# Optimization experiments

Measured on AMD Instinct MI355X. Metric: run time of the kernel, lower is better.

The kernel has to match this reference:

```python
import jax, jax.numpy as jnp
import numpy as np

B, C, W, H = 1024, 1, 128, 128
NUM_IDS = 64
MARGIN = 0.3


def setup_inputs() -> dict:
    key = jax.random.key(0)
    k1, k2 = jax.random.split(key)
    inputs = jax.random.normal(k1, (B, C, W, H), dtype=jnp.float32)
    targets = jax.random.randint(k2, (B,), 0, NUM_IDS, dtype=jnp.int32)
    return {"inputs": inputs, "targets": targets}


def _dc_align(anchor, other):
    # Batched cross-attention alignment (DCModuleOptimized assumption):
    # modi = softmax(anchor @ other^T / sqrt(h)) @ other, per sample.
    h = anchor.shape[-1]
    scale = 1.0 / jnp.sqrt(jnp.asarray(h, anchor.dtype))
    att = jax.nn.softmax(jnp.einsum('bij,bkj->bik', anchor, other) * scale, axis=-1)
    return jnp.einsum('bik,bkj->bij', att, other)


def reference(inputs, targets):
    b, c, w, h = inputs.shape
    x = inputs.reshape(b, -1)                      # (n, d); requires c == 1 downstream
    n = b
    # Pairwise Euclidean distances, stable clamp as in torch code
    sq = jnp.sum(x * x, axis=1)                    # (n,)
    dist = sq[:, None] + sq[None, :] - 2.0 * (x @ x.T)
    dist = jnp.sqrt(jnp.clip(dist, 1e-12, None))   # (n, n)
    mask = targets[:, None] == targets[None, :]    # (n, n) same-identity mask
    # Vectorized hard mining (replaces the per-row Python loop)
    NEG = jnp.asarray(-1e30, dist.dtype)
    POS = jnp.asarray(1e30, dist.dtype)
    hp_idx = jnp.argmax(jnp.where(mask, dist, NEG), axis=1)   # hardest positive per row
    hn_idx = jnp.argmin(jnp.where(mask, POS, dist), axis=1)   # hardest negative per row
    anchor = x.reshape(b, w, h)
    h_pos = anchor[hp_idx]                         # (b, w, h) gathered hard positives
    h_neg = anchor[hn_idx]                         # (b, w, h) gathered hard negatives
    # DC module applied over the whole batch at once
    modi_pos = _dc_align(anchor, h_pos)
    modi_neg = _dc_align(anchor, h_neg)
    dap = anchor.reshape(b, -1) - modi_pos.reshape(b, -1)
    dan = anchor.reshape(b, -1) - modi_neg.reshape(b, -1)
    dist_ap = jnp.sqrt(jnp.sum(dap * dap, axis=1))
    dist_an = jnp.sqrt(jnp.sum(dan * dan, axis=1))
    # MarginRankingLoss with y = 1: mean(relu(dist_ap - dist_an + margin))
    loss = jnp.mean(jax.nn.relu(dist_ap - dist_an + MARGIN))
    return loss
```

## Files before the change

### kernel.cpp

```cpp
#include <hip/hip_runtime.h>
#include <stdint.h>

#define NSAMP 1024
#define D 16384
#define WH 128
#define MARGIN 0.3f
#define SCALE 0.08838834764831845f
#define RSCALE 11.313708498984761f
#define MARG 0.03f
#define NKS 16
#define NTILE 36

typedef unsigned int uint;
typedef unsigned short ushort_t;

typedef __attribute__((ext_vector_type(8))) short bf16x8;
typedef __attribute__((ext_vector_type(4))) float f32x4;

__device__ __forceinline__ float bf2f(unsigned short b) {
    return __uint_as_float(((uint)b) << 16);
}
__device__ __forceinline__ unsigned short f2bf(float f) {
    uint u = __float_as_uint(f);
    u += 0x7fffu + ((u >> 16) & 1u);
    return (unsigned short)(u >> 16);
}
__device__ __forceinline__ void gload_lds16(const void* g, void* l) {
    __builtin_amdgcn_global_load_lds(
        (const __attribute__((address_space(1))) uint32_t*)g,
        (__attribute__((address_space(3))) uint32_t*)l, 16, 0, 0);
}
__device__ __forceinline__ int lds_off(int row, int col) {
    return row * 256 + ((((col >> 3) ^ (row & 15)) << 4) | ((col & 7) << 1));
}

__global__ __launch_bounds__(256) void k_norms_hi(const float* __restrict__ x,
                                                  float* __restrict__ sq,
                                                  ushort_t* __restrict__ xhi) {
    int b = blockIdx.x;
    int tid = threadIdx.x;
    const float* xr = x + (size_t)b * D;
    ushort_t* hr = xhi + (size_t)b * D;
    float s = 0.f;
    #pragma unroll
    for (int m = 0; m < 16; ++m) {
        int e = m * 1024 + tid * 4;
        float4 v = *(const float4*)(xr + e);
        s += v.x * v.x + v.y * v.y + v.z * v.z + v.w * v.w;
        ushort4 h;
        h.x = f2bf(v.x); h.y = f2bf(v.y); h.z = f2bf(v.z); h.w = f2bf(v.w);
        *(ushort4*)(hr + e) = h;
    }
    for (int off = 32; off; off >>= 1) s += __shfl_down(s, off, 64);
    __shared__ float red[4];
    if ((tid & 63) == 0) red[tid >> 6] = s;
    __syncthreads();
    if (tid == 0) sq[b] = red[0] + red[1] + red[2] + red[3];
}

__global__ __launch_bounds__(256) void k_gram_hi(const ushort_t* __restrict__ xhi,
                                                 float* __restrict__ Gp) {
    int n = blockIdx.x;
    int r8 = n & 7;
    int m = n >> 3;
    int h = m / 36;
    int t = m - 36 * h;
    int ks = r8 + 8 * h;
    int bi = 0, rem = t;
    while (rem >= 8 - bi) { rem -= 8 - bi; ++bi; }
    int bj = bi + rem;
    int i0 = bi * 128, j0 = bj * 128;
    int kstart = ks * (D / NKS);

    int tid = threadIdx.x;
    int w = tid >> 6, lane = tid & 63;
    int wm = w & 1, wn = w >> 1;
    int quad = lane >> 4, m16 = lane & 15;
    int srow = lane >> 2, sseg = lane & 3;
    int swseg = sseg ^ ((srow >> 1) & 3);
    int rsw = (quad ^ ((m16 >> 1) & 3)) << 3;

    __shared__ __align__(16) ushort_t A_s[2][128 * 32];
    __shared__ __align__(16) ushort_t B_s[2][128 * 32];

    f32x4 acc[4][4];
    #pragma unroll
    for (int ii = 0; ii < 4; ++ii)
        #pragma unroll
        for (int jj = 0; jj < 4; ++jj)
            acc[ii][jj] = (f32x4){0.f, 0.f, 0.f, 0.f};

    const size_t Abase = (size_t)i0 * D;
    const size_t Bbase = (size_t)j0 * D;

    auto stage = [&](int s) {
        int bsel = s & 1;
        int k0 = kstart + s * 32;
        #pragma unroll
        for (int c = 0; c < 2; ++c) {
            int r = w * 32 + c * 16 + srow;
            size_t go = (size_t)r * D + k0 + swseg * 8;
            int lo = (w * 32 + c * 16) * 32;
            gload_lds16(xhi + Abase + go, &A_s[bsel][lo]);
            gload_lds16(xhi + Bbase + go, &B_s[bsel][lo]);
        }
    };
    auto compute = [&](int bsel) {
        bf16x8 ah[4], bh[4];
        #pragma unroll
        for (int ii = 0; ii < 4; ++ii) {
            int ar = wm * 64 + ii * 16 + m16;
            ah[ii] = *(const bf16x8*)&A_s[bsel][ar * 32 + rsw];
        }
        #pragma unroll
        for (int jj = 0; jj < 4; ++jj) {
            int br = wn * 64 + jj * 16 + m16;
            bh[jj] = *(const bf16x8*)&B_s[bsel][br * 32 + rsw];
        }
        #pragma unroll
        for (int ii = 0; ii < 4; ++ii)
            #pragma unroll
            for (int jj = 0; jj < 4; ++jj)
                acc[ii][jj] = __builtin_amdgcn_mfma_f32_16x16x32_bf16(ah[ii], bh[jj], acc[ii][jj], 0, 0, 0);
    };

    stage(0);
    for (int kb = 0; kb < 31; ++kb) {
        stage(kb + 1);
        asm volatile("s_waitcnt vmcnt(4)" ::: "memory");
        __builtin_amdgcn_sched_barrier(0);
        __builtin_amdgcn_s_barrier();
        compute(kb & 1);
        __builtin_amdgcn_s_barrier();
    }
    asm volatile("s_waitcnt vmcnt(0)" ::: "memory");
    __builtin_amdgcn_sched_barrier(0);
    __builtin_amdgcn_s_barrier();
    compute(1);

    float* Gb = Gp + ((size_t)(t * NKS + ks) << 14);
    #pragma unroll
    for (int ii = 0; ii < 4; ++ii)
        #pragma unroll
        for (int jj = 0; jj < 4; ++jj) {
            int rg = wm * 64 + ii * 16 + quad * 4;
            int cg = wn * 64 + jj * 16 + m16;
            #pragma unroll
            for (int r = 0; r < 4; ++r)
                Gb[(rg + r) * 128 + cg] = acc[ii][jj][r];
        }
}

__global__ __launch_bounds__(256) void k_fold_tri(const float* __restrict__ Gp,
                                                  float* __restrict__ G) {
    int t = blockIdx.x;
    int panel = blockIdx.y;
    int bi = 0, rem = t;
    while (rem >= 8 - bi) { rem -= 8 - bi; ++bi; }
    int bj = bi + rem;
    bool diag = (bi == bj);
    int tid = threadIdx.x;

    const float* P = Gp + (((size_t)t * NKS) << 14) + panel * 4096;

    float4 s[4];
    #pragma unroll
    for (int m = 0; m < 4; ++m)
        s[m] = *(const float4*)(P + (tid + 256 * m) * 4);
    #pragma unroll
    for (int p = 1; p < NKS; ++p) {
        const float* Pp = P + (((size_t)p) << 14);
        #pragma unroll
        for (int m = 0; m < 4; ++m) {
            float4 v = *(const float4*)(Pp + (tid + 256 * m) * 4);
            s[m].x += v.x; s[m].y += v.y; s[m].z += v.z; s[m].w += v.w;
        }
    }

    int i0 = bi * 128, j0 = bj * 128, r0 = panel * 32;
    __shared__ float ts[32][129];
    #pragma unroll
    for (int m = 0; m < 4; ++m) {
        int p4 = (tid + 256 * m) * 4;
        int lr = p4 >> 7, lc = p4 & 127;
        *(float4*)(&G[(size_t)(i0 + r0 + lr) * NSAMP + j0 + lc]) = s[m];
        if (!diag) {
            ts[lr][lc] = s[m].x; ts[lr][lc + 1] = s[m].y;
            ts[lr][lc + 2] = s[m].z; ts[lr][lc + 3] = s[m].w;
        }
    }
    if (diag) return;
    __syncthreads();
    int oc = tid >> 1, half = tid & 1;
    float4 o[4];
    #pragma unroll
    for (int k = 0; k < 4; ++k) {
        int rr = half * 16 + k * 4;
        o[k].x = ts[rr][oc]; o[k].y = ts[rr + 1][oc];
        o[k].z = ts[rr + 2][oc]; o[k].w = ts[rr + 3][oc];
    }
    float* Gm = &G[(size_t)(j0 + oc) * NSAMP + i0 + r0 + half * 16];
    #pragma unroll
    for (int k = 0; k < 4; ++k) *(float4*)(Gm + k * 4) = o[k];
}

__global__ __launch_bounds__(256) void k_select_fix(const float* __restrict__ G,
                                                    const float* __restrict__ sq,
                                                    const int* __restrict__ tgt,
                                                    const float* __restrict__ x,
                                                    const ushort_t* __restrict__ xhi,
                                                    int* __restrict__ hp,
                                                    int* __restrict__ hn,
                                                    float* __restrict__ dsq) {
    int i = blockIdx.x;
    int tid = threadIdx.x;
    float sqi = sq[i];
    int ti = tgt[i];
    float dloc[4]; bool sloc[4];
    float pv = -3.0e38f; int pj = 0x7FFFFFFF;
    float nv = 3.0e38f;  int nj = 0x7FFFFFFF;
    #pragma unroll
    for (int m = 0; m < 4; ++m) {
        int j = tid + 256 * m;
        float g = G[(size_t)i * NSAMP + j];
        float d = sqrtf(fmaxf(sqi + sq[j] - 2.f * g, 1e-12f));
        bool same = (tgt[j] == ti);
        dloc[m] = d; sloc[m] = same;
        float cp = same ? d : -1e30f;
        float cn = same ? 1e30f : d;
        if (cp > pv || (cp == pv && j < pj)) { pv = cp; pj = j; }
        if (cn < nv || (cn == nv && j < nj)) { nv = cn; nj = j; }
    }
    for (int off = 32; off; off >>= 1) {
        float opv = __shfl_down(pv, off, 64); int opj = __shfl_down(pj, off, 64);
        float onv = __shfl_down(nv, off, 64); int onj = __shfl_down(nj, off, 64);
        if (opv > pv || (opv == pv && opj < pj)) { pv = opv; pj = opj; }
        if (onv < nv || (onv == nv && onj < nj)) { nv = onv; nj = onj; }
    }
    __shared__ float spv[4], snv[4];
    __shared__ int spj[4], snj[4];
    __shared__ float bb[2];
    __shared__ int cc[2];
    if ((tid & 63) == 0) { int wv = tid >> 6; spv[wv] = pv; spj[wv] = pj; snv[wv] = nv; snj[wv] = nj; }
    __syncthreads();
    if (tid == 0) {
        for (int wv = 1; wv < 4; ++wv) {
            if (spv[wv] > pv || (spv[wv] == pv && spj[wv] < pj)) { pv = spv[wv]; pj = spj[wv]; }
            if (snv[wv] < nv || (snv[wv] == nv && snj[wv] < nj)) { nv = snv[wv]; nj = snj[wv]; }
        }
        hp[i] = pj; hn[i] = nj;
        dsq[i] = sqi; dsq[NSAMP + i] = sqi;
        bb[0] = pv; bb[1] = nv;
        cc[0] = 0; cc[1] = 0;
    }
    __syncthreads();
    {
        int lp = 0, ln = 0;
        #pragma unroll
        for (int m = 0; m < 4; ++m) {
            if (sloc[m] && dloc[m] >= bb[0] - MARG) lp++;
            if (!sloc[m] && dloc[m] <= bb[1] + MARG) ln++;
        }
        if (lp) atomicAdd(&cc[0], lp);
        if (ln) atomicAdd(&cc[1], ln);
    }
    __syncthreads();

    __shared__ int cand[32];
    __shared__ int ncand;
    __shared__ float bred[4];
    const float* xi = x + (size_t)i * D;
    const ushort_t* hi = xhi + (size_t)i * D;
    for (int type = 0; type < 2; ++type) {
        if (cc[type] <= 1) continue;
        if (tid == 0) ncand = 0;
        __syncthreads();
        float bd = bb[type];
        #pragma unroll
        for (int m = 0; m < 4; ++m) {
            int j = tid + 256 * m;
            bool fl = (type == 0) ? (sloc[m] && dloc[m] >= bd - MARG)
                                  : (!sloc[m] && dloc[m] <= bd + MARG);
            if (fl) { int k = atomicAdd(&ncand, 1); if (k < 32) cand[k] = j; }
        }
        __syncthreads();
        int nc = ncand < 32 ? ncand : 32;
        float bestv = (type == 0) ? -3.0e38f : 3.0e38f;
        int bestj = 0x7FFFFFFF;
        for (int c = 0; c < nc; ++c) {
            int j = cand[c];
            const float* xj = x + (size_t)j * D;
            const ushort_t* hj = xhi + (size_t)j * D;
            float corr = 0.f;
            #pragma unroll
            for (int m = 0; m < 16; ++m) {
                int k = m * 1024 + tid * 4;
                float4 xa = *(const float4*)(xi + k);
                float4 xb = *(const float4*)(xj + k);
                ushort4 ha = *(const ushort4*)(hi + k);
                ushort4 hb = *(const ushort4*)(hj + k);
                float a0 = bf2f(ha.x), a1 = bf2f(ha.y), a2 = bf2f(ha.z), a3 = bf2f(ha.w);
                float b0 = bf2f(hb.x), b1 = bf2f(hb.y), b2 = bf2f(hb.z), b3 = bf2f(hb.w);
                corr += a0 * (xb.x - b0) + (xa.x - a0) * b0;
                corr += a1 * (xb.y - b1) + (xa.y - a1) * b1;
                corr += a2 * (xb.z - b2) + (xa.z - a2) * b2;
                corr += a3 * (xb.w - b3) + (xa.w - a3) * b3;
            }
            for (int off = 32; off; off >>= 1) corr += __shfl_down(corr, off, 64);
            if ((tid & 63) == 0) bred[tid >> 6] = corr;
            __syncthreads();
            float cs = bred[0] + bred[1] + bred[2] + bred[3];
            float g = G[(size_t)i * NSAMP + j];
            float d2 = sqi + sq[j] - 2.f * (g + cs);
            float d = sqrtf(fmaxf(d2, 1e-12f));
            if (type == 0) {
                if (d > bestv || (d == bestv && j < bestj)) { bestv = d; bestj = j; }
            } else {
                if (d < bestv || (d == bestv && j < bestj)) { bestv = d; bestj = j; }
            }
            __syncthreads();
        }
        if (tid == 0 && nc > 0) { if (type == 0) hp[i] = bestj; else hn[i] = bestj; }
        __syncthreads();
    }
}

__global__ __launch_bounds__(256) void k_dc_mfma(const ushort_t* __restrict__ xhi,
                                                 const int* __restrict__ hp,
                                                 const int* __restrict__ hn,
                                                 float* __restrict__ dsq) {
    int b = blockIdx.x;
    int which = blockIdx.y;
    int oidx = (which == 0) ? hp[b] : hn[b];
    const ushort_t* Ag = xhi + (size_t)b * D;
    const ushort_t* Og = xhi + (size_t)oidx * D;

    __shared__ __align__(16) char smem[32768];

    int tid = threadIdx.x;
    int wv = tid >> 6, lane = tid & 63;
    int quad = lane >> 4, m16 = lane & 15;

    bf16x8 af[2][4];
    #pragma unroll
    for (int h = 0; h < 2; ++h) {
        int rt = h * 4 + wv;
        #pragma unroll
        for (int ks = 0; ks < 4; ++ks)
            af[h][ks] = *(const bf16x8*)(Ag + (rt * 16 + m16) * WH + ks * 32 + quad * 8);
    }

    {
        uint4 stg[8];
        #pragma unroll
        for (int k = 0; k < 8; ++k)
            stg[k] = *(const uint4*)((const char*)Og + (size_t)(tid + 256 * k) * 16);
        #pragma unroll
        for (int k = 0; k < 8; ++k) {
            int g = tid + 256 * k;
            *(uint4*)(smem + lds_off(g >> 4, (g & 15) * 8)) = stg[k];
        }
    }
    __syncthreads();

    f32x4 acc[2][8];
    #pragma unroll
    for (int h = 0; h < 2; ++h)
        #pragma unroll
        for (int ti = 0; ti < 8; ++ti)
            acc[h][ti] = (f32x4){0.f, 0.f, 0.f, 0.f};
    #pragma unroll
    for (int ks = 0; ks < 4; ++ks) {
        bf16x8 of[8];
        #pragma unroll
        for (int ti = 0; ti < 8; ++ti)
            of[ti] = *(const bf16x8*)(smem + lds_off(ti * 16 + m16, (ks * 4 + quad) * 8));
        #pragma unroll
        for (int h = 0; h < 2; ++h)
            #pragma unroll
            for (int ti = 0; ti < 8; ++ti)
                acc[h][ti] = __builtin_amdgcn_mfma_f32_16x16x32_bf16(of[ti], af[h][ks], acc[h][ti], 0, 0, 0);
    }

    int c0 = (tid & 31) * 4, h0 = (tid >> 5) * 16;
    uint4 trd[4][2];
    #pragma unroll
    for (int j = 0; j < 4; ++j)
        #pragma unroll
        for (int k = 0; k < 2; ++k)
            trd[j][k] = *(const uint4*)(smem + lds_off(c0 + j, h0 + 8 * k));
    __syncthreads();

    #pragma unroll
    for (int i = 0; i < 16; ++i) {
        uint v[4];
        #pragma unroll
        for (int j = 0; j < 4; ++j) {
            uint wo = ((const uint*)&trd[j][i >> 3])[(i >> 1) & 3];
            v[j] = (i & 1) ? (wo >> 16) : (wo & 0xffffu);
        }
        uint2 pk;
        pk.x = v[0] | (v[1] << 16);
        pk.y = v[2] | (v[3] << 16);
        *(uint2*)(smem + lds_off(h0 + i, c0)) = pk;
    }

    float tpart[2];
    bf16x8 pf[2][4];
    #pragma unroll
    for (int h = 0; h < 2; ++h) {
        float mx = -3.0e38f;
        #pragma unroll
        for (int ti = 0; ti < 8; ++ti)
            #pragma unroll
            for (int r = 0; r < 4; ++r) {
                float s = acc[h][ti][r] * SCALE;
                acc[h][ti][r] = s;
                mx = fmaxf(mx, s);
            }
        mx = fmaxf(mx, __shfl_xor(mx, 16, 64));
        mx = fmaxf(mx, __shfl_xor(mx, 32, 64));
        float sum = 0.f, tnum = 0.f;
        #pragma unroll
        for (int ti = 0; ti < 8; ++ti)
            #pragma unroll
            for (int r = 0; r < 4; ++r) {
                float s = acc[h][ti][r];
                float e = __expf(s - mx);
                acc[h][ti][r] = e;
                sum += e;
                tnum += s * e;
            }
        sum += __shfl_xor(sum, 16, 64);
        sum += __shfl_xor(sum, 32, 64);
        tnum += __shfl_xor(tnum, 16, 64);
        tnum += __shfl_xor(tnum, 32, 64);
        float inv = 1.f / sum;
        tpart[h] = 0.25f * tnum * inv;

        uint Ep[8][2];
        #pragma unroll
        for (int ti = 0; ti < 8; ++ti) {
            Ep[ti][0] = (uint)f2bf(acc[h][ti][0] * inv) |
                        ((uint)f2bf(acc[h][ti][1] * inv) << 16);
            Ep[ti][1] = (uint)f2bf(acc[h][ti][2] * inv) |
                        ((uint)f2bf(acc[h][ti][3] * inv) << 16);
        }
        int tih = quad >> 1;
        #pragma unroll
        for (int ks = 0; ks < 4; ++ks) {
            union { uint u[4]; bf16x8 v; } fr;
            #pragma unroll
            for (int k = 0; k < 4; ++k) {
                int src = (((quad << 1) + (k >> 1)) & 3) * 16 + m16;
                int a = __shfl((int)Ep[2 * ks + 0][k & 1], src, 64);
                int bsh = __shfl((int)Ep[2 * ks + 1][k & 1], src, 64);
                fr.u[k] = (uint)((tih == 0) ? a : bsh);
            }
            pf[h][ks] = fr.v;
        }
    }
    __syncthreads();

    #pragma unroll
    for (int h = 0; h < 2; ++h)
        #pragma unroll
        for (int tj = 0; tj < 8; ++tj)
            acc[h][tj] = (f32x4){0.f, 0.f, 0.f, 0.f};
    #pragma unroll
    for (int ks = 0; ks < 4; ++ks) {
        bf16x8 otf[8];
        #pragma unroll
        for (int tj = 0; tj < 8; ++tj)
            otf[tj] = *(const bf16x8*)(smem + lds_off(tj * 16 + m16, (ks * 4 + quad) * 8));
        #pragma unroll
        for (int h = 0; h < 2; ++h)
            #pragma unroll
            for (int tj = 0; tj < 8; ++tj)
                acc[h][tj] = __builtin_amdgcn_mfma_f32_16x16x32_bf16(pf[h][ks], otf[tj], acc[h][tj], 0, 0, 0);
    }

    float part = 0.f;
    #pragma unroll
    for (int h = 0; h < 2; ++h) {
        float m2 = 0.f;
        #pragma unroll
        for (int tj = 0; tj < 8; ++tj)
            #pragma unroll
            for (int r = 0; r < 4; ++r) {
                float mvv = acc[h][tj][r];
                m2 += mvv * mvv;
            }
        part += m2 - 2.f * RSCALE * tpart[h];
    }
    for (int off = 32; off; off >>= 1) part += __shfl_down(part, off, 64);
    if (lane == 0) atomicAdd(&dsq[which * NSAMP + b], part);
}

__global__ void k_loss(const float* __restrict__ dsq, float* __restrict__ out) {
    int tid = threadIdx.x;
    float s = 0.f;
    #pragma unroll
    for (int m = 0; m < 4; ++m) {
        int b = tid + 256 * m;
        float ap = sqrtf(fmaxf(dsq[b], 0.f));
        float an = sqrtf(fmaxf(dsq[NSAMP + b], 0.f));
        s += fmaxf(ap - an + MARGIN, 0.f);
    }
    for (int off = 32; off; off >>= 1) s += __shfl_down(s, off, 64);
    __shared__ float red[4];
    if ((tid & 63) == 0) red[tid >> 6] = s;
    __syncthreads();
    if (tid == 0) out[0] = (red[0] + red[1] + red[2] + red[3]) * (1.f / NSAMP);
}

extern "C" void kernel_launch(void* const* d_in, const int* in_sizes, int n_in,
                              void* d_out, int out_size, void* d_ws, size_t ws_size,
                              hipStream_t stream) {
    const float* x = (const float*)d_in[0];
    const int* tgt = (const int*)d_in[1];
    float* out = (float*)d_out;
    char* ws = (char*)d_ws;

    const size_t GPB = (size_t)NTILE * NKS * 65536;
    const size_t XB = (size_t)NSAMP * D * 2;
    const size_t GB1 = (size_t)NSAMP * NSAMP * 4;

    float* Gp = (float*)ws;
    ushort_t* xhi = (ushort_t*)(ws + GPB);
    float* G = (float*)(ws + GPB + XB);
    char* tail = ws + GPB + XB + GB1;
    float* sq = (float*)tail;
    float* dsq = sq + NSAMP;
    int* hp = (int*)(dsq + 2 * NSAMP);
    int* hn = hp + NSAMP;

    k_norms_hi<<<NSAMP, 256, 0, stream>>>(x, sq, xhi);
    k_gram_hi<<<NKS * NTILE, 256, 0, stream>>>(xhi, Gp);
    k_fold_tri<<<dim3(NTILE, 4), 256, 0, stream>>>(Gp, G);
    k_select_fix<<<NSAMP, 256, 0, stream>>>(G, sq, tgt, x, xhi, hp, hn, dsq);
    k_dc_mfma<<<dim3(NSAMP, 2), 256, 0, stream>>>(xhi, hp, hn, dsq);
    k_loss<<<1, 256, 0, stream>>>(dsq, out);
}
```

Baseline: 195.0 us.

## Fuse pos/neg DC alignment into one block and simplify gram pipeline

The DC alignment kernel now handles both the hardest-positive and the hardest-negative partner in one block. The anchor fragments are loaded once and reused, and the partner tile is staged directly into LDS with async global-to-LDS loads. The gram kernel's double-buffered loop is rewritten to use plain __syncthreads instead of explicit vmcnt waits, and both kernels raise wave priority around MFMA bursts with s_setprio. This halves the DC grid and removes redundant anchor loads, but the two partners are now processed serially within a block, so there is less parallelism. The gram loop may also lose some of its overlap between loads and compute.

```diff
diff --git a/kernel.cpp b/kernel.cpp
--- a/kernel.cpp
+++ b/kernel.cpp
@@ -93,9 +93,7 @@
     const size_t Abase = (size_t)i0 * D;
     const size_t Bbase = (size_t)j0 * D;
 
-    auto stage = [&](int s) {
-        int bsel = s & 1;
-        int k0 = kstart + s * 32;
+    auto stage = [&](int bsel, int k0) {
         #pragma unroll
         for (int c = 0; c < 2; ++c) {
             int r = w * 32 + c * 16 + srow;
@@ -117,26 +115,24 @@
             int br = wn * 64 + jj * 16 + m16;
             bh[jj] = *(const bf16x8*)&B_s[bsel][br * 32 + rsw];
         }
+        __builtin_amdgcn_s_setprio(1);
         #pragma unroll
         for (int ii = 0; ii < 4; ++ii)
             #pragma unroll
             for (int jj = 0; jj < 4; ++jj)
                 acc[ii][jj] = __builtin_amdgcn_mfma_f32_16x16x32_bf16(ah[ii], bh[jj], acc[ii][jj], 0, 0, 0);
+        __builtin_amdgcn_s_setprio(0);
     };
 
-    stage(0);
-    for (int kb = 0; kb < 31; ++kb) {
-        stage(kb + 1);
-        asm volatile("s_waitcnt vmcnt(4)" ::: "memory");
-        __builtin_amdgcn_sched_barrier(0);
-        __builtin_amdgcn_s_barrier();
-        compute(kb & 1);
-        __builtin_amdgcn_s_barrier();
-    }
-    asm volatile("s_waitcnt vmcnt(0)" ::: "memory");
-    __builtin_amdgcn_sched_barrier(0);
-    __builtin_amdgcn_s_barrier();
-    compute(1);
+    stage(0, kstart);
+    __syncthreads();
+    int buf = 0;
+    for (int kb = 0; kb < 32; ++kb) {
+        if (kb < 31) stage(buf ^ 1, kstart + (kb + 1) * 32);
+        compute(buf);
+        __syncthreads();
+        buf ^= 1;
+    }
 
     float* Gb = Gp + ((size_t)(t * NKS + ks) << 14);
     #pragma unroll
@@ -330,10 +326,8 @@
                                                  const int* __restrict__ hn,
                                                  float* __restrict__ dsq) {
     int b = blockIdx.x;
-    int which = blockIdx.y;
-    int oidx = (which == 0) ? hp[b] : hn[b];
     const ushort_t* Ag = xhi + (size_t)b * D;
-    const ushort_t* Og = xhi + (size_t)oidx * D;
+    int oidx[2] = {hp[b], hn[b]};
 
     __shared__ __align__(16) char smem[32768];
 
@@ -350,151 +344,163 @@
             af[h][ks] = *(const bf16x8*)(Ag + (rt * 16 + m16) * WH + ks * 32 + quad * 8);
     }
 
-    {
-        uint4 stg[8];
-        #pragma unroll
-        for (int k = 0; k < 8; ++k)
-            stg[k] = *(const uint4*)((const char*)Og + (size_t)(tid + 256 * k) * 16);
+    auto stage_O = [&](const ushort_t* Og) {
         #pragma unroll
         for (int k = 0; k < 8; ++k) {
-            int g = tid + 256 * k;
-            *(uint4*)(smem + lds_off(g >> 4, (g & 15) * 8)) = stg[k];
-        }
-    }
-    __syncthreads();
-
-    f32x4 acc[2][8];
-    #pragma unroll
-    for (int h = 0; h < 2; ++h)
-        #pragma unroll
-        for (int ti = 0; ti < 8; ++ti)
-            acc[h][ti] = (f32x4){0.f, 0.f, 0.f, 0.f};
-    #pragma unroll
-    for (int ks = 0; ks < 4; ++ks) {
-        bf16x8 of[8];
-        #pragma unroll
-        for (int ti = 0; ti < 8; ++ti)
-            of[ti] = *(const bf16x8*)(smem + lds_off(ti * 16 + m16, (ks * 4 + quad) * 8));
+            int p = tid + 256 * k;
+            int row = p >> 4, s = p & 15;
+            gload_lds16(Og + row * 128 + ((s ^ (row & 15)) << 3),
+                        smem + p * 16);
+        }
+    };
+
+    stage_O(xhi + (size_t)oidx[0] * D);
+    __syncthreads();
+
+    for (int which = 0; which < 2; ++which) {
+        f32x4 acc[2][8];
         #pragma unroll
         for (int h = 0; h < 2; ++h)
             #pragma unroll
             for (int ti = 0; ti < 8; ++ti)
-                acc[h][ti] = __builtin_amdgcn_mfma_f32_16x16x32_bf16(of[ti], af[h][ks], acc[h][ti], 0, 0, 0);
-    }
-
-    int c0 = (tid & 31) * 4, h0 = (tid >> 5) * 16;
-    uint4 trd[4][2];
-    #pragma unroll
-    for (int j = 0; j < 4; ++j)
-        #pragma unroll
-        for (int k = 0; k < 2; ++k)
-            trd[j][k] = *(const uint4*)(smem + lds_off(c0 + j, h0 + 8 * k));
-    __syncthreads();
-
-    #pragma unroll
-    for (int i = 0; i < 16; ++i) {
-        uint v[4];
-        #pragma unroll
-        for (int j = 0; j < 4; ++j) {
-            uint wo = ((const uint*)&trd[j][i >> 3])[(i >> 1) & 3];
-            v[j] = (i & 1) ? (wo >> 16) : (wo & 0xffffu);
-        }
-        uint2 pk;
-        pk.x = v[0] | (v[1] << 16);
-        pk.y = v[2] | (v[3] << 16);
-        *(uint2*)(smem + lds_off(h0 + i, c0)) = pk;
-    }
-
-    float tpart[2];
-    bf16x8 pf[2][4];
-    #pragma unroll
-    for (int h = 0; h < 2; ++h) {
-        float mx = -3.0e38f;
-        #pragma unroll
-        for (int ti = 0; ti < 8; ++ti)
-            #pragma unroll
-            for (int r = 0; r < 4; ++r) {
-                float s = acc[h][ti][r] * SCALE;
-                acc[h][ti][r] = s;
-                mx = fmaxf(mx, s);
+                acc[h][ti] = (f32x4){0.f, 0.f, 0.f, 0.f};
+        #pragma unroll
+        for (int ks = 0; ks < 4; ++ks) {
+            bf16x8 of[8];
+            #pragma unroll
+            for (int ti = 0; ti < 8; ++ti)
+                of[ti] = *(const bf16x8*)(smem + lds_off(ti * 16 + m16, (ks * 4 + quad) * 8));
+            __builtin_amdgcn_s_setprio(1);
+            #pragma unroll
+            for (int h = 0; h < 2; ++h)
+                #pragma unroll
+                for (int ti = 0; ti < 8; ++ti)
+                    acc[h][ti] = __builtin_amdgcn_mfma_f32_16x16x32_bf16(of[ti], af[h][ks], acc[h][ti], 0, 0, 0);
+            __builtin_amdgcn_s_setprio(0);
+        }
+
+        int c0 = (tid & 31) * 4, h0 = (tid >> 5) * 16;
+        uint4 trd[4][2];
+        #pragma unroll
+        for (int j = 0; j < 4; ++j)
+            #pragma unroll
+            for (int k = 0; k < 2; ++k)
+                trd[j][k] = *(const uint4*)(smem + lds_off(c0 + j, h0 + 8 * k));
+        __syncthreads();
+
+        #pragma unroll
+        for (int i = 0; i < 16; ++i) {
+            uint v[4];
+            #pragma unroll
+            for (int j = 0; j < 4; ++j) {
+                uint wo = ((const uint*)&trd[j][i >> 3])[(i >> 1) & 3];
+                v[j] = (i & 1) ? (wo >> 16) : (wo & 0xffffu);
             }
-        mx = fmaxf(mx, __shfl_xor(mx, 16, 64));
-        mx = fmaxf(mx, __shfl_xor(mx, 32, 64));
-        float sum = 0.f, tnum = 0.f;
-        #pragma unroll
-        for (int ti = 0; ti < 8; ++ti)
-            #pragma unroll
-            for (int r = 0; r < 4; ++r) {
-                float s = acc[h][ti][r];
-                float e = __expf(s - mx);
-                acc[h][ti][r] = e;
-                sum += e;
-                tnum += s * e;
+            uint2 pk;
+            pk.x = v[0] | (v[1] << 16);
+            pk.y = v[2] | (v[3] << 16);
+            *(uint2*)(smem + lds_off(h0 + i, c0)) = pk;
+        }
+
+        float tpart[2];
+        bf16x8 pf[2][4];
+        #pragma unroll
+        for (int h = 0; h < 2; ++h) {
+            float mx = -3.0e38f;
+            #pragma unroll
+            for (int ti = 0; ti < 8; ++ti)
+                #pragma unroll
+                for (int r = 0; r < 4; ++r) {
+                    float s = acc[h][ti][r] * SCALE;
+                    acc[h][ti][r] = s;
+                    mx = fmaxf(mx, s);
+                }
+            mx = fmaxf(mx, __shfl_xor(mx, 16, 64));
+            mx = fmaxf(mx, __shfl_xor(mx, 32, 64));
+            float sum = 0.f, tnum = 0.f;
+            #pragma unroll
+            for (int ti = 0; ti < 8; ++ti)
+                #pragma unroll
+                for (int r = 0; r < 4; ++r) {
+                    float s = acc[h][ti][r];
+                    float e = __expf(s - mx);
+                    acc[h][ti][r] = e;
+                    sum += e;
+                    tnum += s * e;
+                }
+            sum += __shfl_xor(sum, 16, 64);
+            sum += __shfl_xor(sum, 32, 64);
+            tnum += __shfl_xor(tnum, 16, 64);
+            tnum += __shfl_xor(tnum, 32, 64);
+            float inv = 1.f / sum;
+            tpart[h] = 0.25f * tnum * inv;
+
+            uint Ep[8][2];
+            #pragma unroll
+            for (int ti = 0; ti < 8; ++ti) {
+                Ep[ti][0] = (uint)f2bf(acc[h][ti][0] * inv) |
+                            ((uint)f2bf(acc[h][ti][1] * inv) << 16);
+                Ep[ti][1] = (uint)f2bf(acc[h][ti][2] * inv) |
+                            ((uint)f2bf(acc[h][ti][3] * inv) << 16);
             }
-        sum += __shfl_xor(sum, 16, 64);
-        sum += __shfl_xor(sum, 32, 64);
-        tnum += __shfl_xor(tnum, 16, 64);
-        tnum += __shfl_xor(tnum, 32, 64);
-        float inv = 1.f / sum;
-        tpart[h] = 0.25f * tnum * inv;
-
-        uint Ep[8][2];
-        #pragma unroll
-        for (int ti = 0; ti < 8; ++ti) {
-            Ep[ti][0] = (uint)f2bf(acc[h][ti][0] * inv) |
-                        ((uint)f2bf(acc[h][ti][1] * inv) << 16);
-            Ep[ti][1] = (uint)f2bf(acc[h][ti][2] * inv) |
-                        ((uint)f2bf(acc[h][ti][3] * inv) << 16);
-        }
-        int tih = quad >> 1;
+            int tih = quad >> 1;
+            #pragma unroll
+            for (int ks = 0; ks < 4; ++ks) {
+                union { uint u[4]; bf16x8 v; } fr;
+                #pragma unroll
+                for (int k = 0; k < 4; ++k) {
+                    int src = (((quad << 1) + (k >> 1)) & 3) * 16 + m16;
+                    int a = __shfl((int)Ep[2 * ks + 0][k & 1], src, 64);
+                    int bsh = __shfl((int)Ep[2 * ks + 1][k & 1], src, 64);
+                    fr.u[k] = (uint)((tih == 0) ? a : bsh);
+                }
+                pf[h][ks] = fr.v;
+            }
+        }
+        __syncthreads();
+
+        #pragma unroll
+        for (int h = 0; h < 2; ++h)
+            #pragma unroll
+            for (int tj = 0; tj < 8; ++tj)
+                acc[h][tj] = (f32x4){0.f, 0.f, 0.f, 0.f};
         #pragma unroll
         for (int ks = 0; ks < 4; ++ks) {
-            union { uint u[4]; bf16x8 v; } fr;
-            #pragma unroll
-            for (int k = 0; k < 4; ++k) {
-                int src = (((quad << 1) + (k >> 1)) & 3) * 16 + m16;
-                int a = __shfl((int)Ep[2 * ks + 0][k & 1], src, 64);
-                int bsh = __shfl((int)Ep[2 * ks + 1][k & 1], src, 64);
-                fr.u[k] = (uint)((tih == 0) ? a : bsh);
-            }
-            pf[h][ks] = fr.v;
-        }
-    }
-    __syncthreads();
-
-    #pragma unroll
-    for (int h = 0; h < 2; ++h)
-        #pragma unroll
-        for (int tj = 0; tj < 8; ++tj)
-            acc[h][tj] = (f32x4){0.f, 0.f, 0.f, 0.f};
-    #pragma unroll
-    for (int ks = 0; ks < 4; ++ks) {
-        bf16x8 otf[8];
-        #pragma unroll
-        for (int tj = 0; tj < 8; ++tj)
-            otf[tj] = *(const bf16x8*)(smem + lds_off(tj * 16 + m16, (ks * 4 + quad) * 8));
-        #pragma unroll
-        for (int h = 0; h < 2; ++h)
+            bf16x8 otf[8];
             #pragma unroll
             for (int tj = 0; tj < 8; ++tj)
-                acc[h][tj] = __builtin_amdgcn_mfma_f32_16x16x32_bf16(pf[h][ks], otf[tj], acc[h][tj], 0, 0, 0);
-    }
-
-    float part = 0.f;
-    #pragma unroll
-    for (int h = 0; h < 2; ++h) {
-        float m2 = 0.f;
-        #pragma unroll
-        for (int tj = 0; tj < 8; ++tj)
-            #pragma unroll
-            for (int r = 0; r < 4; ++r) {
-                float mvv = acc[h][tj][r];
-                m2 += mvv * mvv;
-            }
-        part += m2 - 2.f * RSCALE * tpart[h];
-    }
-    for (int off = 32; off; off >>= 1) part += __shfl_down(part, off, 64);
-    if (lane == 0) atomicAdd(&dsq[which * NSAMP + b], part);
+                otf[tj] = *(const bf16x8*)(smem + lds_off(tj * 16 + m16, (ks * 4 + quad) * 8));
+            __builtin_amdgcn_s_setprio(1);
+            #pragma unroll
+            for (int h = 0; h < 2; ++h)
+                #pragma unroll
+                for (int tj = 0; tj < 8; ++tj)
+                    acc[h][tj] = __builtin_amdgcn_mfma_f32_16x16x32_bf16(pf[h][ks], otf[tj], acc[h][tj], 0, 0, 0);
+            __builtin_amdgcn_s_setprio(0);
+        }
+
+        float part = 0.f;
+        #pragma unroll
+        for (int h = 0; h < 2; ++h) {
+            float m2 = 0.f;
+            #pragma unroll
+            for (int tj = 0; tj < 8; ++tj)
+                #pragma unroll
+                for (int r = 0; r < 4; ++r) {
+                    float mvv = acc[h][tj][r];
+                    m2 += mvv * mvv;
+                }
+            part += m2 - 2.f * RSCALE * tpart[h];
+        }
+        for (int off = 32; off; off >>= 1) part += __shfl_down(part, off, 64);
+        if (lane == 0) atomicAdd(&dsq[which * NSAMP + b], part);
+
+        if (which == 0) {
+            __syncthreads();
+            stage_O(xhi + (size_t)oidx[1] * D);
+            __syncthreads();
+        }
+    }
 }
 
 __global__ void k_loss(const float* __restrict__ dsq, float* __restrict__ out) {
@@ -539,6 +545,6 @@
     k_gram_hi<<<NKS * NTILE, 256, 0, stream>>>(xhi, Gp);
     k_fold_tri<<<dim3(NTILE, 4), 256, 0, stream>>>(Gp, G);
     k_select_fix<<<NSAMP, 256, 0, stream>>>(G, sq, tgt, x, xhi, hp, hn, dsq);
-    k_dc_mfma<<<dim3(NSAMP, 2), 256, 0, stream>>>(xhi, hp, hn, dsq);
+    k_dc_mfma<<<NSAMP, 256, 0, stream>>>(xhi, hp, hn, dsq);
     k_loss<<<1, 256, 0, stream>>>(dsq, out);
 }
```

Result: slower. 204.5 us (+4.9%).
